# Performance work log

Measured on AMD Instinct MI355X. Metric: run time of the kernel, lower is better.

Reference implementation:

```python
import jax, jax.numpy as jnp
import numpy as np

K_TOP = 32
TEMPERATURE = 0.1
EPS = 1e-12  # torch F.normalize eps


def _l2_normalize(x):
    n = jnp.linalg.norm(x, axis=-1, keepdims=True)
    return x / jnp.maximum(n, EPS)


def setup_inputs() -> dict:
    key = jax.random.key(0)
    kq, kk, kv = jax.random.split(key, 3)
    B, T, d_k, d_v, N = 4, 512, 512, 512, 65536
    queries = jax.random.normal(kq, (B, T, d_k), dtype=jnp.float32)
    keys = jax.random.normal(kk, (N, d_k), dtype=jnp.float32)
    values = jax.random.normal(kv, (N, d_v), dtype=jnp.float32)
    return {"queries": queries, "keys": keys, "values": values}


def reference(queries, keys, values):
    B, T, d_k = queries.shape
    d_v = values.shape[1]
    flat_q = queries.reshape(B * T, d_k)
    qn = _l2_normalize(flat_q)           # [BT, d_k]
    kn = _l2_normalize(keys)             # [N, d_k]
    scores = qn @ kn.T                   # [BT, N] cosine similarities
    topk_scores, topk_idx = jax.lax.top_k(scores, K_TOP)  # [BT, K]
    attn = jax.nn.softmax(topk_scores / TEMPERATURE, axis=-1)  # [BT, K]
    retrieved = values[topk_idx]         # [BT, K, d_v]
    aggregated = jnp.einsum('nk,nkd->nd', attn, retrieved)  # [BT, d_v]
    return (aggregated.reshape(B, T, d_v),
            attn.reshape(B, T, K_TOP),
            topk_idx.reshape(B, T, K_TOP))
```

## Files before the change

### kernel.cpp

```cpp
#include <hip/hip_runtime.h>
#include <math.h>

#define M_ROWS 2048
#define N_KEYS 65536
#define DKK 512
#define DVV 512
#define KTOP 32
#define NSPLIT 16
#define NRANGE (N_KEYS / NSPLIT)
#define BM 128
#define BN 128
#define MBLKS (M_ROWS / BM)
#define NTILES (NRANGE / BN)
#define KSTEPS (DKK / 32)
#define TOT (NTILES * KSTEPS)
#define CAP 16
#define CSTR 17
#define TILE_E 4096

typedef _Float16 f16x8 __attribute__((ext_vector_type(8)));
typedef float f32x4 __attribute__((ext_vector_type(4)));


__global__ void __launch_bounds__(256) norm_split_kernel(
    const float* __restrict__ q, const float* __restrict__ keys,
    _Float16* __restrict__ QhT, _Float16* __restrict__ QlT,
    _Float16* __restrict__ KhT, _Float16* __restrict__ KlT) {
  const int gw = (blockIdx.x * 256 + threadIdx.x) >> 6;
  const int lane = threadIdx.x & 63;
  const float* row; _Float16 *oh, *ol; int rr;
  if (gw < M_ROWS) {
    row = q + (size_t)gw * DKK; rr = gw & 127;
    const size_t tb = (size_t)(gw >> 7) * 16 * TILE_E;
    oh = QhT + tb; ol = QlT + tb;
  } else {
    const int n = gw - M_ROWS;
    if (n >= N_KEYS) return;
    row = keys + (size_t)n * DKK; rr = n & 127;
    const size_t tb = (size_t)(n >> 7) * 16 * TILE_E;
    oh = KhT + tb; ol = KlT + tb;
  }
  const float4 a = *(const float4*)&row[lane * 8];
  const float4 b = *(const float4*)&row[lane * 8 + 4];
  float s = a.x*a.x + a.y*a.y + a.z*a.z + a.w*a.w
          + b.x*b.x + b.y*b.y + b.z*b.z + b.w*b.w;
#pragma unroll
  for (int off = 32; off; off >>= 1) s += __shfl_xor(s, off);
  const float inv = 1.0f / fmaxf(sqrtf(s), 1e-12f);

  f16x8 h, l;
  const float e[8] = {a.x, a.y, a.z, a.w, b.x, b.y, b.z, b.w};
#pragma unroll
  for (int j = 0; j < 8; ++j) {
    const float y = e[j] * inv;
    h[j] = (_Float16)y;
    l[j] = (_Float16)(y - (float)h[j]);
  }
  const int ks = lane >> 2, oct = lane & 3;
  const int po = oct ^ ((rr >> 1) & 3);
  const size_t off = (size_t)ks * TILE_E + rr * 32 + po * 8;
  *(f16x8*)&oh[off] = h;
  *(f16x8*)&ol[off] = l;
}

__device__ __forceinline__ void insert32(float* tS, int* tI, float s, int idx) {
  const float ms = tS[31]; const int mi_ = tI[31];
  if (s < ms || (s == ms && idx > mi_)) return;
  int p = 0;
  while (p < KTOP && (tS[p] > s || (tS[p] == s && tI[p] < idx))) ++p;
  for (int qq = KTOP - 1; qq > p; --qq) { tS[qq] = tS[qq-1]; tI[qq] = tI[qq-1]; }
  tS[p] = s; tI[p] = idx;
}

__device__ __forceinline__ void gll16(const _Float16* g, _Float16* l) {
  __builtin_amdgcn_global_load_lds(
      (const __attribute__((address_space(1))) void*)g,
      (__attribute__((address_space(3))) void*)l, 16, 0, 0);
}

#define SQL(i) sQl##i
#define SKH(i) sKh##i
#define SKL(i) sKl##i

#define STAGE(B, KB, KS2) do {                                         \
  gll16(QlT + qlb + (size_t)(KS2) * TILE_E, &SQL(B)[ldsA]);            \
  gll16(KhT + (KB) + (size_t)(KS2) * TILE_E, &SKH(B)[ldsA]);           \
  gll16(KlT + (KB) + (size_t)(KS2) * TILE_E, &SKL(B)[ldsA]);           \
} while (0)

#define KBAR(NVM) do {                                                 \
  __builtin_amdgcn_sched_barrier(0);                                   \
  asm volatile("s_waitcnt vmcnt(" #NVM ")" ::: "memory");              \
  __builtin_amdgcn_sched_barrier(0);                                   \
  __builtin_amdgcn_s_barrier();                                        \
  __builtin_amdgcn_sched_barrier(0);                                   \
} while (0)

#define LBAR() do {                                                    \
  __builtin_amdgcn_sched_barrier(0);                                   \
  asm volatile("s_waitcnt lgkmcnt(0)" ::: "memory");                   \
  __builtin_amdgcn_sched_barrier(0);                                   \
  __builtin_amdgcn_s_barrier();                                        \
  __builtin_amdgcn_sched_barrier(0);                                   \
} while (0)

#define ONESTEP(KS, RB, SB) do {                                       \
  if (lastct && (KS) == 14) { KBAR(3); }                               \
  else if (lastct && (KS) == 15) { KBAR(0); }                          \
  else { KBAR(6); }                                                    \
  if ((KS) < 13) { STAGE(SB, kb, (KS) + 3); }                          \
  else if (!lastct) { STAGE(SB, kb + 16 * TILE_E, (KS) - 13); }        \
  f16x8 Al_[2], Bh_[4], Bl_[4];                                        \
  Al_[0] = *(const f16x8*)&SQL(RB)[offA[0]];                           \
  Al_[1] = *(const f16x8*)&SQL(RB)[offA[1]];                           \
  _Pragma("unroll")                                                    \
  for (int ni = 0; ni < 4; ++ni) {                                     \
    Bh_[ni] = *(const f16x8*)&SKH(RB)[offB[ni]];                       \
    Bl_[ni] = *(const f16x8*)&SKL(RB)[offB[ni]];                       \
  }                                                                    \
  __builtin_amdgcn_s_setprio(1);                                       \
  _Pragma("unroll")                                                    \
  for (int mi = 0; mi < 2; ++mi) {                                     \
    const f16x8 qa = (mi == 0) ? qh0[KS] : qh1[KS];                    \
    _Pragma("unroll")                                                  \
    for (int ni = 0; ni < 4; ++ni) {                                   \
      acc[mi][ni] = __builtin_amdgcn_mfma_f32_16x16x32_f16(Al_[mi], Bh_[ni], acc[mi][ni], 0, 0, 0); \
      acc[mi][ni] = __builtin_amdgcn_mfma_f32_16x16x32_f16(qa, Bl_[ni], acc[mi][ni], 0, 0, 0);      \
      acc[mi][ni] = __builtin_amdgcn_mfma_f32_16x16x32_f16(qa, Bh_[ni], acc[mi][ni], 0, 0, 0);      \
    }                                                                  \
  }                                                                    \
  __builtin_amdgcn_s_setprio(0);                                       \
} while (0)

__global__ void __launch_bounds__(512, 2) gemm_topk_kernel(
    const _Float16* __restrict__ QhT, const _Float16* __restrict__ QlT,
    const _Float16* __restrict__ KhT, const _Float16* __restrict__ KlT,
    float* __restrict__ pscore, int* __restrict__ pidx) {
  __shared__ __attribute__((aligned(16))) _Float16 sQl0[TILE_E], sQl1[TILE_E], sQl2[TILE_E], sQl3[TILE_E];
  __shared__ __attribute__((aligned(16))) _Float16 sKh0[TILE_E], sKh1[TILE_E], sKh2[TILE_E], sKh3[TILE_E];
  __shared__ __attribute__((aligned(16))) _Float16 sKl0[TILE_E], sKl1[TILE_E], sKl2[TILE_E], sKl3[TILE_E];
  __shared__ float topS[BM * 33];
  __shared__ int   topI[BM * 33];
  __shared__ float candS[BM * CSTR];
  __shared__ int   candI[BM * CSTR];
  __shared__ float mS[BM];
  __shared__ int   cnt[BM];
  __shared__ int   sOver;

  const int tid  = threadIdx.x;
  const int lane = tid & 63;
  const int w    = tid >> 6;
  const int wr   = w >> 1, wc = w & 1;
  const int cl   = lane & 15;
  const int g    = lane >> 4;
  const int g4   = g * 4;

  const int lin   = (int)(blockIdx.x + gridDim.x * blockIdx.y);
  const int virt  = (lin & 7) * 32 + (lin >> 3);
  const int mblk  = virt & (MBLKS - 1);
  const int split = virt >> 4;
  const int qbase  = mblk * BM;
  const int nbase0 = split * NRANGE;

  const int ldsA = tid * 8;
  const size_t qlb = (size_t)mblk * 16 * TILE_E + ldsA;
  const size_t kb0 = (size_t)(split * NTILES) * 16 * TILE_E + ldsA;

  int offA[2], offB[4];
#pragma unroll
  for (int mi = 0; mi < 2; ++mi) {
    const int r = wr * 32 + mi * 16 + cl;
    offA[mi] = r * 32 + (g ^ ((r >> 1) & 3)) * 8;
  }
#pragma unroll
  for (int ni = 0; ni < 4; ++ni) {
    const int c = wc * 64 + ni * 16 + cl;
    offB[ni] = c * 32 + (g ^ ((c >> 1) & 3)) * 8;
  }

  f16x8 qh0[16], qh1[16];
  {
    const size_t qhb = (size_t)mblk * 16 * TILE_E;
#pragma unroll
    for (int ks = 0; ks < 16; ++ks) {
      qh0[ks] = *(const f16x8*)&QhT[qhb + (size_t)ks * TILE_E + offA[0]];
      qh1[ks] = *(const f16x8*)&QhT[qhb + (size_t)ks * TILE_E + offA[1]];
    }
  }

  if (tid < BM) {
    mS[tid] = -INFINITY; cnt[tid] = 0;
#pragma unroll
    for (int j = 0; j < KTOP; ++j) { topS[tid*33+j] = -INFINITY; topI[tid*33+j] = 0x7fffffff; }
  }
  if (tid == 0) sOver = 0;

  STAGE(0, kb0, 0);
  STAGE(1, kb0, 1);
  STAGE(2, kb0, 2);

  for (int ct = 0; ct < NTILES; ++ct) {
    const bool lastct = (ct == NTILES - 1);
    const size_t kb = kb0 + (size_t)ct * 16 * TILE_E;
    const int n0 = nbase0 + ct * BN;
    f32x4 acc[2][4];
#pragma unroll
    for (int mi = 0; mi < 2; ++mi)
#pragma unroll
      for (int ni = 0; ni < 4; ++ni) acc[mi][ni] = (f32x4)0.0f;

    ONESTEP(0, 0, 3);  ONESTEP(1, 1, 0);  ONESTEP(2, 2, 1);  ONESTEP(3, 3, 2);
    ONESTEP(4, 0, 3);  ONESTEP(5, 1, 0);  ONESTEP(6, 2, 1);  ONESTEP(7, 3, 2);
    ONESTEP(8, 0, 3);  ONESTEP(9, 1, 0);  ONESTEP(10, 2, 1); ONESTEP(11, 3, 2);
    ONESTEP(12, 0, 3); ONESTEP(13, 1, 0); ONESTEP(14, 2, 1); ONESTEP(15, 3, 2);

    LBAR();
    float m[2][4];
#pragma unroll
    for (int mi = 0; mi < 2; ++mi) {
      const f32x4 mv = *(const f32x4*)&mS[wr * 32 + mi * 16 + g4];
      m[mi][0] = mv[0]; m[mi][1] = mv[1]; m[mi][2] = mv[2]; m[mi][3] = mv[3];
    }
    unsigned int pend = 0u;
#pragma unroll
    for (int mi = 0; mi < 2; ++mi)
#pragma unroll
      for (int ni = 0; ni < 4; ++ni)
#pragma unroll
        for (int j = 0; j < 4; ++j)
          if (acc[mi][ni][j] >= m[mi][j])
            pend |= 1u << (mi * 16 + ni * 4 + j);

    for (;;) {
      if (pend) {
#pragma unroll
        for (int mi = 0; mi < 2; ++mi)
#pragma unroll
          for (int ni = 0; ni < 4; ++ni)
#pragma unroll
            for (int j = 0; j < 4; ++j) {
              const int bit = mi * 16 + ni * 4 + j;
              if (pend & (1u << bit)) {
                const int r = wr * 32 + mi * 16 + g4 + j;
                const int t = atomicAdd(&cnt[r], 1);
                if (t < CAP) {
                  candS[r * CSTR + t] = acc[mi][ni][j];
                  candI[r * CSTR + t] = n0 + wc * 64 + ni * 16 + cl;
                  pend &= ~(1u << bit);
                }
              }
            }
      }
      LBAR();
      if (tid < BM) {
        int nc = cnt[tid];
        if (nc > CAP) { sOver = 1; nc = CAP; }
        float* tS = &topS[tid * 33];
        int*   tI = &topI[tid * 33];
        for (int e = 0; e < nc; ++e) insert32(tS, tI, candS[tid * CSTR + e], candI[tid * CSTR + e]);
        mS[tid] = tS[KTOP - 1];
        cnt[tid] = 0;
      }
      LBAR();
      const int over = sOver;
      LBAR();
      if (tid == 0) sOver = 0;
      if (!over) break;
#pragma unroll
      for (int mi = 0; mi < 2; ++mi) {
        const f32x4 mv = *(const f32x4*)&mS[wr * 32 + mi * 16 + g4];
        m[mi][0] = mv[0]; m[mi][1] = mv[1]; m[mi][2] = mv[2]; m[mi][3] = mv[3];
      }
      unsigned int keep = 0u;
#pragma unroll
      for (int mi = 0; mi < 2; ++mi)
#pragma unroll
        for (int ni = 0; ni < 4; ++ni)
#pragma unroll
          for (int j = 0; j < 4; ++j) {
            const int bit = mi * 16 + ni * 4 + j;
            if ((pend & (1u << bit)) && acc[mi][ni][j] >= m[mi][j])
              keep |= 1u << bit;
          }
      pend = keep;
    }
  }

  if (tid < BM) {
    const size_t base = ((size_t)(qbase + tid) * NSPLIT + split) * KTOP;
    for (int j = 0; j < KTOP; ++j) {
      pscore[base + j] = topS[tid * 33 + j];
      pidx[base + j]   = topI[tid * 33 + j];
    }
  }
}


#define QB 128
#define NB 128
#define KC 32
#define FNTILES (NRANGE / NB)
#define KCH (DKK / KC)
#define LDST 132

__global__ void __launch_bounds__(256) norm_kernel(
    const float* __restrict__ q, const float* __restrict__ keys,
    float* __restrict__ qn, float* __restrict__ kinv) {
  const int gw = (blockIdx.x * 256 + threadIdx.x) >> 6;
  const int lane = threadIdx.x & 63;
  if (gw < M_ROWS) {
    const float* row = q + (size_t)gw * DKK;
    float4 a = ((const float4*)row)[lane];
    float4 b = ((const float4*)row)[lane + 64];
    float s = a.x*a.x + a.y*a.y + a.z*a.z + a.w*a.w
            + b.x*b.x + b.y*b.y + b.z*b.z + b.w*b.w;
#pragma unroll
    for (int off = 32; off; off >>= 1) s += __shfl_xor(s, off);
    const float inv = 1.0f / fmaxf(sqrtf(s), 1e-12f);
    float* orow = qn + (size_t)gw * DKK;
    ((float4*)orow)[lane]      = make_float4(a.x*inv, a.y*inv, a.z*inv, a.w*inv);
    ((float4*)orow)[lane + 64] = make_float4(b.x*inv, b.y*inv, b.z*inv, b.w*inv);
  } else {
    const int n = gw - M_ROWS;
    if (n < N_KEYS) {
      const float* row = keys + (size_t)n * DKK;
      float4 a = ((const float4*)row)[lane];
      float4 b = ((const float4*)row)[lane + 64];
      float s = a.x*a.x + a.y*a.y + a.z*a.z + a.w*a.w
              + b.x*b.x + b.y*b.y + b.z*b.z + b.w*b.w;
#pragma unroll
      for (int off = 32; off; off >>= 1) s += __shfl_xor(s, off);
      if (lane == 0) kinv[n] = 1.0f / fmaxf(sqrtf(s), 1e-12f);
    }
  }
}

__device__ __forceinline__ void lds_wr_tile(float* dst, int k8, int r, float4 v, float scale) {
  dst[(k8 * 4 + 0) * LDST + r] = v.x * scale;
  dst[(k8 * 4 + 1) * LDST + r] = v.y * scale;
  dst[(k8 * 4 + 2) * LDST + r] = v.z * scale;
  dst[(k8 * 4 + 3) * LDST + r] = v.w * scale;
}

__global__ void __launch_bounds__(256, 1) score_topk_kernel(
    const float* __restrict__ qn, const float* __restrict__ keys,
    const float* __restrict__ kinv,
    float* __restrict__ pscore, int* __restrict__ pidx) {
  __shared__ float u[16896];
  __shared__ float topS[QB * KTOP];
  __shared__ int   topI[QB * KTOP];

  const int tid = threadIdx.x;
  const int tx = tid & 15, ty = tid >> 4;
  const int qbase = blockIdx.y * QB;
  const int nbase0 = blockIdx.x * NRANGE;

  for (int i = tid; i < QB * KTOP; i += 256) { topS[i] = -INFINITY; topI[i] = 0; }
  __syncthreads();

  for (int t = 0; t < FNTILES; ++t) {
    const int n0 = nbase0 + t * NB;
    float acc[8][8];
#pragma unroll
    for (int i = 0; i < 8; ++i)
#pragma unroll
      for (int j = 0; j < 8; ++j) acc[i][j] = 0.0f;

#pragma unroll
    for (int p = 0; p < 4; ++p) {
      const int id = tid + p * 256;
      const int r = id >> 3, k8 = id & 7;
      const float4 va = *(const float4*)&qn[(size_t)(qbase + r) * DKK + k8 * 4];
      const float4 vb = *(const float4*)&keys[(size_t)(n0 + r) * DKK + k8 * 4];
      const float kv = kinv[n0 + r];
      lds_wr_tile(u, k8, r, va, 1.0f);
      lds_wr_tile(u + 4224, k8, r, vb, kv);
    }
    __syncthreads();

    for (int kc = 0; kc < KCH; ++kc) {
      float4 pa[4], pb[4]; float pk[4];
      const bool pre = (kc + 1 < KCH);
      if (pre) {
#pragma unroll
        for (int p = 0; p < 4; ++p) {
          const int id = tid + p * 256;
          const int r = id >> 3, k8 = id & 7;
          pa[p] = *(const float4*)&qn[(size_t)(qbase + r) * DKK + (kc + 1) * KC + k8 * 4];
          pb[p] = *(const float4*)&keys[(size_t)(n0 + r) * DKK + (kc + 1) * KC + k8 * 4];
          pk[p] = kinv[n0 + r];
        }
      }
      const float* As = u + (kc & 1) * 8448;
      const float* Bs = As + 4224;
#pragma unroll 4
      for (int kk = 0; kk < KC; ++kk) {
        const float4 a0 = *(const float4*)&As[kk * LDST + ty * 4];
        const float4 a1 = *(const float4*)&As[kk * LDST + ty * 4 + 64];
        const float4 b0 = *(const float4*)&Bs[kk * LDST + tx * 4];
        const float4 b1 = *(const float4*)&Bs[kk * LDST + tx * 4 + 64];
        const float av[8] = {a0.x,a0.y,a0.z,a0.w,a1.x,a1.y,a1.z,a1.w};
        const float bv[8] = {b0.x,b0.y,b0.z,b0.w,b1.x,b1.y,b1.z,b1.w};
#pragma unroll
        for (int i = 0; i < 8; ++i)
#pragma unroll
          for (int j = 0; j < 8; ++j)
            acc[i][j] = fmaf(av[i], bv[j], acc[i][j]);
      }
      if (pre) {
        float* Ad = u + ((kc + 1) & 1) * 8448;
        float* Bd = Ad + 4224;
#pragma unroll
        for (int p = 0; p < 4; ++p) {
          const int id = tid + p * 256;
          const int r = id >> 3, k8 = id & 7;
          lds_wr_tile(Ad, k8, r, pa[p], 1.0f);
          lds_wr_tile(Bd, k8, r, pb[p], pk[p]);
        }
      }
      __syncthreads();
    }

#pragma unroll
    for (int ib = 0; ib < 2; ++ib)
#pragma unroll
      for (int i = 0; i < 4; ++i) {
        const int r = ty * 4 + i + ib * 64;
#pragma unroll
        for (int jb = 0; jb < 2; ++jb) {
          *(float4*)&u[r * LDST + tx * 4 + jb * 64] =
              make_float4(acc[ib*4+i][jb*4+0], acc[ib*4+i][jb*4+1],
                          acc[ib*4+i][jb*4+2], acc[ib*4+i][jb*4+3]);
        }
      }
    __syncthreads();

    if (tid < QB) {
      const int row = tid;
      float* tS = &topS[row * KTOP];
      int*   tI = &topI[row * KTOP];
      float mSv = tS[KTOP - 1]; int mIv = tI[KTOP - 1];
      for (int c4 = 0; c4 < NB / 4; ++c4) {
        const float4 v = *(const float4*)&u[row * LDST + c4 * 4];
#pragma unroll
        for (int wv = 0; wv < 4; ++wv) {
          const float s = (&v.x)[wv];
          const int idx = n0 + c4 * 4 + wv;
          if (s > mSv || (s == mSv && idx < mIv)) {
            int p = 0;
            while (p < KTOP && (tS[p] > s || (tS[p] == s && tI[p] < idx))) ++p;
            for (int qq = KTOP - 1; qq > p; --qq) { tS[qq] = tS[qq-1]; tI[qq] = tI[qq-1]; }
            tS[p] = s; tI[p] = idx;
            mSv = tS[KTOP - 1]; mIv = tI[KTOP - 1];
          }
        }
      }
    }
    __syncthreads();
  }

  if (tid < QB) {
    const size_t base = ((size_t)(qbase + tid) * NSPLIT + blockIdx.x) * KTOP;
    for (int j = 0; j < KTOP; ++j) {
      pscore[base + j] = topS[tid * KTOP + j];
      pidx[base + j]   = topI[tid * KTOP + j];
    }
  }
}

__global__ void __launch_bounds__(256) merge_kernel(
    const float* __restrict__ pscore, const int* __restrict__ pidx,
    const float* __restrict__ values,
    float* __restrict__ out_agg, float* __restrict__ out_attn, float* __restrict__ out_idx) {
  __shared__ float attn_s[KTOP];
  __shared__ int   sel_i[KTOP];
  const int row = blockIdx.x;
  const int tid = threadIdx.x;

  if (tid < 64) {
    const int lane = tid;
    const float* ps = pscore + (size_t)row * NSPLIT * KTOP;
    const int*   pi = pidx   + (size_t)row * NSPLIT * KTOP;
    int pos = 0;
    float s; int idx;
    if (lane < NSPLIT) { s = ps[lane * KTOP]; idx = pi[lane * KTOP]; }
    else { s = -INFINITY; idx = 0x7fffffff; }
    for (int it = 0; it < KTOP; ++it) {
      float wsv = s; int wi = idx; int wl = lane;
#pragma unroll
      for (int off = 32; off; off >>= 1) {
        const float os = __shfl_xor(wsv, off);
        const int   oi = __shfl_xor(wi, off);
        const int   ol = __shfl_xor(wl, off);
        if (os > wsv || (os == wsv && oi < wi)) { wsv = os; wi = oi; wl = ol; }
      }
      if (lane == 0) { attn_s[it] = wsv; sel_i[it] = wi; }
      if (lane == wl) {
        ++pos;
        if (pos < KTOP) { s = ps[lane * KTOP + pos]; idx = pi[lane * KTOP + pos]; }
        else { s = -INFINITY; idx = 0x7fffffff; }
      }
    }
  }
  __syncthreads();
  if (tid < KTOP) {
    const float mm = attn_s[0];
    const float e = expf((attn_s[tid] - mm) * 10.0f);
    float tsum = e;
#pragma unroll
    for (int off = 16; off; off >>= 1) tsum += __shfl_xor(tsum, off);
    const float a = e / tsum;
    out_attn[(size_t)row * KTOP + tid] = a;
    out_idx [(size_t)row * KTOP + tid] = (float)sel_i[tid];
    attn_s[tid] = a;
  }
  __syncthreads();

  const int d = tid * 2;
  float2 accv = make_float2(0.0f, 0.0f);
  for (int j = 0; j < KTOP; ++j) {
    const float wgt = attn_s[j];
    const float2 v = *(const float2*)&values[(size_t)sel_i[j] * DVV + d];
    accv.x = fmaf(wgt, v.x, accv.x);
    accv.y = fmaf(wgt, v.y, accv.y);
  }
  *(float2*)&out_agg[(size_t)row * DVV + d] = accv;
}

extern "C" void kernel_launch(void* const* d_in, const int* in_sizes, int n_in,
                              void* d_out, int out_size, void* d_ws, size_t ws_size,
                              hipStream_t stream) {
  const float* q      = (const float*)d_in[0];
  const float* keys   = (const float*)d_in[1];
  const float* values = (const float*)d_in[2];

  float* out      = (float*)d_out;
  float* out_agg  = out;
  float* out_attn = out + (size_t)M_ROWS * DVV;
  float* out_idx  = out_attn + (size_t)M_ROWS * KTOP;

  const size_t needFast =
      (size_t)M_ROWS * DKK * 2 * 2
    + (size_t)N_KEYS * DKK * 2 * 2
    + (size_t)M_ROWS * NSPLIT * KTOP * 8;

  if (ws_size >= needFast) {
    _Float16* QhT = (_Float16*)d_ws;
    _Float16* QlT = QhT + (size_t)M_ROWS * DKK;
    _Float16* KhT = QlT + (size_t)M_ROWS * DKK;
    _Float16* KlT = KhT + (size_t)N_KEYS * DKK;
    float* pscore = (float*)(KlT + (size_t)N_KEYS * DKK);
    int*   pidx   = (int*)(pscore + (size_t)M_ROWS * NSPLIT * KTOP);

    norm_split_kernel<<<(M_ROWS + N_KEYS) / 4, 256, 0, stream>>>(q, keys, QhT, QlT, KhT, KlT);
    dim3 g2(MBLKS, NSPLIT, 1);
    gemm_topk_kernel<<<g2, 512, 0, stream>>>(QhT, QlT, KhT, KlT, pscore, pidx);
    merge_kernel<<<M_ROWS, 256, 0, stream>>>(pscore, pidx, values, out_agg, out_attn, out_idx);
  } else {
    float* ws     = (float*)d_ws;
    float* qn     = ws;
    float* kinv   = qn + (size_t)M_ROWS * DKK;
    float* pscore = kinv + N_KEYS;
    int*   pidx   = (int*)(pscore + (size_t)M_ROWS * NSPLIT * KTOP);

    norm_kernel<<<(M_ROWS + N_KEYS) / 4, 256, 0, stream>>>(q, keys, qn, kinv);
    dim3 g2(NSPLIT, M_ROWS / QB, 1);
    score_topk_kernel<<<g2, 256, 0, stream>>>(qn, keys, kinv, pscore, pidx);
    merge_kernel<<<M_ROWS, 256, 0, stream>>>(pscore, pidx, values, out_agg, out_attn, out_idx);
  }
}
```

Before: 1.928 ms.

## Stream Qh through LDS with a 3-stage ring buffer instead of registers

```diff
diff --git a/kernel.cpp b/kernel.cpp
--- a/kernel.cpp
+++ b/kernel.cpp
@@ -78,67 +78,38 @@
       (__attribute__((address_space(3))) void*)l, 16, 0, 0);
 }
 
-#define SQL(i) sQl##i
-#define SKH(i) sKh##i
-#define SKL(i) sKl##i
-
-#define STAGE(B, KB, KS2) do {                                         \
-  gll16(QlT + qlb + (size_t)(KS2) * TILE_E, &SQL(B)[ldsA]);            \
-  gll16(KhT + (KB) + (size_t)(KS2) * TILE_E, &SKH(B)[ldsA]);           \
-  gll16(KlT + (KB) + (size_t)(KS2) * TILE_E, &SKL(B)[ldsA]);           \
+__device__ __forceinline__ f16x8 ldsr128(const _Float16* p) {
+  f16x8 d;
+  const __attribute__((address_space(3))) _Float16* lp =
+      (const __attribute__((address_space(3))) _Float16*)p;
+  asm volatile("ds_read_b128 %0, %1" : "=v"(d) : "v"(lp));
+  return d;
+}
+
+#define STAGE(RBS, SG, QKS) do {                                       \
+  const size_t _qo = qb + (size_t)(QKS) * TILE_E;                      \
+  const size_t _ko = kb0 + (size_t)(SG) * TILE_E;                      \
+  gll16(QhT + _qo, &sQh[RBS][ldsA]);                                   \
+  gll16(QlT + _qo, &sQl[RBS][ldsA]);                                   \
+  gll16(KhT + _ko, &sKh[RBS][ldsA]);                                   \
+  gll16(KlT + _ko, &sKl[RBS][ldsA]);                                   \
 } while (0)
 
-#define KBAR(NVM) do {                                                 \
-  __builtin_amdgcn_sched_barrier(0);                                   \
-  asm volatile("s_waitcnt vmcnt(" #NVM ")" ::: "memory");              \
-  __builtin_amdgcn_sched_barrier(0);                                   \
-  __builtin_amdgcn_s_barrier();                                        \
-  __builtin_amdgcn_sched_barrier(0);                                   \
-} while (0)
+#define SB0() __builtin_amdgcn_sched_barrier(0)
 
 #define LBAR() do {                                                    \
-  __builtin_amdgcn_sched_barrier(0);                                   \
-  asm volatile("s_waitcnt lgkmcnt(0)" ::: "memory");                   \
-  __builtin_amdgcn_sched_barrier(0);                                   \
-  __builtin_amdgcn_s_barrier();                                        \
-  __builtin_amdgcn_sched_barrier(0);                                   \
-} while (0)
-
-#define ONESTEP(KS, RB, SB) do {                                       \
-  if (lastct && (KS) == 14) { KBAR(3); }                               \
-  else if (lastct && (KS) == 15) { KBAR(0); }                          \
-  else { KBAR(6); }                                                    \
-  if ((KS) < 13) { STAGE(SB, kb, (KS) + 3); }                          \
-  else if (!lastct) { STAGE(SB, kb + 16 * TILE_E, (KS) - 13); }        \
-  f16x8 Al_[2], Bh_[4], Bl_[4];                                        \
-  Al_[0] = *(const f16x8*)&SQL(RB)[offA[0]];                           \
-  Al_[1] = *(const f16x8*)&SQL(RB)[offA[1]];                           \
-  _Pragma("unroll")                                                    \
-  for (int ni = 0; ni < 4; ++ni) {                                     \
-    Bh_[ni] = *(const f16x8*)&SKH(RB)[offB[ni]];                       \
-    Bl_[ni] = *(const f16x8*)&SKL(RB)[offB[ni]];                       \
-  }                                                                    \
-  __builtin_amdgcn_s_setprio(1);                                       \
-  _Pragma("unroll")                                                    \
-  for (int mi = 0; mi < 2; ++mi) {                                     \
-    const f16x8 qa = (mi == 0) ? qh0[KS] : qh1[KS];                    \
-    _Pragma("unroll")                                                  \
-    for (int ni = 0; ni < 4; ++ni) {                                   \
-      acc[mi][ni] = __builtin_amdgcn_mfma_f32_16x16x32_f16(Al_[mi], Bh_[ni], acc[mi][ni], 0, 0, 0); \
-      acc[mi][ni] = __builtin_amdgcn_mfma_f32_16x16x32_f16(qa, Bl_[ni], acc[mi][ni], 0, 0, 0);      \
-      acc[mi][ni] = __builtin_amdgcn_mfma_f32_16x16x32_f16(qa, Bh_[ni], acc[mi][ni], 0, 0, 0);      \
-    }                                                                  \
-  }                                                                    \
-  __builtin_amdgcn_s_setprio(0);                                       \
+  SB0(); asm volatile("s_waitcnt lgkmcnt(0)" ::: "memory");            \
+  SB0(); __builtin_amdgcn_s_barrier(); SB0();                          \
 } while (0)
 
 __global__ void __launch_bounds__(512, 2) gemm_topk_kernel(
     const _Float16* __restrict__ QhT, const _Float16* __restrict__ QlT,
     const _Float16* __restrict__ KhT, const _Float16* __restrict__ KlT,
     float* __restrict__ pscore, int* __restrict__ pidx) {
-  __shared__ __attribute__((aligned(16))) _Float16 sQl0[TILE_E], sQl1[TILE_E], sQl2[TILE_E], sQl3[TILE_E];
-  __shared__ __attribute__((aligned(16))) _Float16 sKh0[TILE_E], sKh1[TILE_E], sKh2[TILE_E], sKh3[TILE_E];
-  __shared__ __attribute__((aligned(16))) _Float16 sKl0[TILE_E], sKl1[TILE_E], sKl2[TILE_E], sKl3[TILE_E];
+  __shared__ __attribute__((aligned(16))) _Float16 sQh[3][TILE_E];
+  __shared__ __attribute__((aligned(16))) _Float16 sQl[3][TILE_E];
+  __shared__ __attribute__((aligned(16))) _Float16 sKh[3][TILE_E];
+  __shared__ __attribute__((aligned(16))) _Float16 sKl[3][TILE_E];
   __shared__ float topS[BM * 33];
   __shared__ int   topI[BM * 33];
   __shared__ float candS[BM * CSTR];
@@ -163,7 +134,7 @@
   const int nbase0 = split * NRANGE;
 
   const int ldsA = tid * 8;
-  const size_t qlb = (size_t)mblk * 16 * TILE_E + ldsA;
+  const size_t qb  = (size_t)mblk * 16 * TILE_E + ldsA;
   const size_t kb0 = (size_t)(split * NTILES) * 16 * TILE_E + ldsA;
 
   int offA[2], offB[4];
@@ -178,16 +149,6 @@
     offB[ni] = c * 32 + (g ^ ((c >> 1) & 3)) * 8;
   }
 
-  f16x8 qh0[16], qh1[16];
-  {
-    const size_t qhb = (size_t)mblk * 16 * TILE_E;
-#pragma unroll
-    for (int ks = 0; ks < 16; ++ks) {
-      qh0[ks] = *(const f16x8*)&QhT[qhb + (size_t)ks * TILE_E + offA[0]];
-      qh1[ks] = *(const f16x8*)&QhT[qhb + (size_t)ks * TILE_E + offA[1]];
-    }
-  }
-
   if (tid < BM) {
     mS[tid] = -INFINITY; cnt[tid] = 0;
 #pragma unroll
@@ -195,13 +156,12 @@
   }
   if (tid == 0) sOver = 0;
 
-  STAGE(0, kb0, 0);
-  STAGE(1, kb0, 1);
-  STAGE(2, kb0, 2);
+  STAGE(0, 0, 0);
+  STAGE(1, 1, 1);
+
+  int rb = 0;
 
   for (int ct = 0; ct < NTILES; ++ct) {
-    const bool lastct = (ct == NTILES - 1);
-    const size_t kb = kb0 + (size_t)ct * 16 * TILE_E;
     const int n0 = nbase0 + ct * BN;
     f32x4 acc[2][4];
 #pragma unroll
@@ -209,10 +169,49 @@
 #pragma unroll
       for (int ni = 0; ni < 4; ++ni) acc[mi][ni] = (f32x4)0.0f;
 
-    ONESTEP(0, 0, 3);  ONESTEP(1, 1, 0);  ONESTEP(2, 2, 1);  ONESTEP(3, 3, 2);
-    ONESTEP(4, 0, 3);  ONESTEP(5, 1, 0);  ONESTEP(6, 2, 1);  ONESTEP(7, 3, 2);
-    ONESTEP(8, 0, 3);  ONESTEP(9, 1, 0);  ONESTEP(10, 2, 1); ONESTEP(11, 3, 2);
-    ONESTEP(12, 0, 3); ONESTEP(13, 1, 0); ONESTEP(14, 2, 1); ONESTEP(15, 3, 2);
+    for (int ks = 0; ks < KSTEPS; ++ks) {
+      const int s = ct * KSTEPS + ks;
+      if (s == TOT - 1) {
+        SB0(); asm volatile("s_waitcnt vmcnt(0)" ::: "memory"); SB0();
+      } else {
+        SB0(); asm volatile("s_waitcnt vmcnt(4)" ::: "memory"); SB0();
+      }
+      __builtin_amdgcn_s_barrier();
+      SB0();
+
+      if (s + 2 < TOT) {
+        int rb2 = rb + 2; if (rb2 >= 3) rb2 -= 3;
+        STAGE(rb2, s + 2, (s + 2) & 15);
+      }
+      SB0();
+
+      f16x8 Ah0 = ldsr128(&sQh[rb][offA[0]]);
+      f16x8 Ah1 = ldsr128(&sQh[rb][offA[1]]);
+      f16x8 Al0 = ldsr128(&sQl[rb][offA[0]]);
+      f16x8 Al1 = ldsr128(&sQl[rb][offA[1]]);
+      f16x8 Bh[4], Bl[4];
+#pragma unroll
+      for (int ni = 0; ni < 4; ++ni) {
+        Bh[ni] = ldsr128(&sKh[rb][offB[ni]]);
+        Bl[ni] = ldsr128(&sKl[rb][offB[ni]]);
+      }
+      asm volatile("s_waitcnt lgkmcnt(0)" ::: "memory");
+      SB0();
+
+      __builtin_amdgcn_s_setprio(1);
+#pragma unroll
+      for (int ni = 0; ni < 4; ++ni) {
+        acc[0][ni] = __builtin_amdgcn_mfma_f32_16x16x32_f16(Al0, Bh[ni], acc[0][ni], 0, 0, 0);
+        acc[0][ni] = __builtin_amdgcn_mfma_f32_16x16x32_f16(Ah0, Bl[ni], acc[0][ni], 0, 0, 0);
+        acc[0][ni] = __builtin_amdgcn_mfma_f32_16x16x32_f16(Ah0, Bh[ni], acc[0][ni], 0, 0, 0);
+        acc[1][ni] = __builtin_amdgcn_mfma_f32_16x16x32_f16(Al1, Bh[ni], acc[1][ni], 0, 0, 0);
+        acc[1][ni] = __builtin_amdgcn_mfma_f32_16x16x32_f16(Ah1, Bl[ni], acc[1][ni], 0, 0, 0);
+        acc[1][ni] = __builtin_amdgcn_mfma_f32_16x16x32_f16(Ah1, Bh[ni], acc[1][ni], 0, 0, 0);
+      }
+      __builtin_amdgcn_s_setprio(0);
+
+      ++rb; if (rb >= 3) rb -= 3;
+    }
 
     LBAR();
     float m[2][4];
```

Result: faster. 1.704 ms (-11.6%).
